# Kernel tuning notes

Measured on AMD Instinct MI355X. Metric: run time of the kernel, lower is better.

The kernel has to match this reference:

```python
import jax, jax.numpy as jnp
import numpy as np

B, S, T, D, H, HD = 1, 2048, 256, 3072, 24, 128
FF = 4 * D
EPS_LN = 1e-6
EPS_RMS = 1e-6


def _layernorm(x):
    m = jnp.mean(x, axis=-1, keepdims=True)
    v = jnp.mean(jnp.square(x - m), axis=-1, keepdims=True)
    return (x - m) * jax.lax.rsqrt(v + EPS_LN)


def _rmsnorm(x, w):
    return x * jax.lax.rsqrt(jnp.mean(jnp.square(x), axis=-1, keepdims=True) + EPS_RMS) * w


def _rope_interleaved(x, cos, sin):
    # x: [B,S,H,HD], cos/sin: [S,HD//2]; non-neox (interleaved) style
    x1 = x[..., 0::2]
    x2 = x[..., 1::2]
    c = cos[None, :, None, :]
    s = sin[None, :, None, :]
    o1 = x1 * c - x2 * s
    o2 = x2 * c + x1 * s
    return jnp.stack([o1, o2], axis=-1).reshape(x.shape)


def setup_inputs() -> dict:
    key = jax.random.key(0)
    ks = jax.random.split(key, 12)

    def n(k, shape, scale):
        return jax.random.normal(k, shape, dtype=jnp.float32) * scale

    # real RoPE tables
    pos = np.arange(S, dtype=np.float64)
    inv_freq = 1.0 / (10000.0 ** (np.arange(0, HD, 2, dtype=np.float64) / HD))
    ang = np.outer(pos, inv_freq)  # [S, HD//2]

    return {
        "img": n(ks[0], (B, S, D), 1.0),
        "vec": n(ks[1], (B, D), 1.0),
        "cos": jnp.asarray(np.cos(ang), jnp.float32),
        "sin": jnp.asarray(np.sin(ang), jnp.float32),
        "k_txt": n(ks[2], (B, T, H, HD), 1.0),
        "v_txt": n(ks[3], (B, T, H, HD), 1.0),
        "mod_w": n(ks[4], (D, 6 * D), 0.02),
        "mod_b": jnp.zeros((6 * D,), jnp.float32),
        "qkv_w": n(ks[5], (D, 3 * D), 0.02),
        "qkv_b": jnp.zeros((3 * D,), jnp.float32),
        "qn_w": jnp.ones((HD,), jnp.float32),
        "kn_w": jnp.ones((HD,), jnp.float32),
        "proj_w": n(ks[6], (D, D), 0.02),
        "proj_b": jnp.zeros((D,), jnp.float32),
        "mlp_w1": n(ks[7], (D, FF), 0.02),
        "mlp_b1": jnp.zeros((FF,), jnp.float32),
        "mlp_w2": n(ks[8], (FF, D), 0.02),
        "mlp_b2": jnp.zeros((D,), jnp.float32),
    }


def reference(img, vec, cos, sin, k_txt, v_txt, mod_w, mod_b, qkv_w, qkv_b,
              qn_w, kn_w, proj_w, proj_b, mlp_w1, mlp_b1, mlp_w2, mlp_b2):
    # modulation: silu(vec) -> linear -> 6 chunks, each [B,1,D]
    mod = jax.nn.silu(vec) @ mod_w + mod_b
    (a_shift, a_scale, a_gate, m_shift, m_scale, m_gate) = [
        m[:, None, :] for m in jnp.split(mod, 6, axis=-1)
    ]

    # LayerNorm (no affine) + scale/shift modulate
    x = _layernorm(img) * (1.0 + a_scale) + a_shift

    qkv = (x @ qkv_w + qkv_b).reshape(B, S, 3, H, HD)
    q, k, v = qkv[:, :, 0], qkv[:, :, 1], qkv[:, :, 2]
    q = _rmsnorm(q, qn_w)
    k = _rmsnorm(k, kn_w)
    q = _rope_interleaved(q, cos, sin)
    k = _rope_interleaved(k, cos, sin)

    # concat text KV cache (no RoPE on text tokens)
    k_all = jnp.concatenate([k, k_txt], axis=1)  # [B,S+T,H,HD]
    v_all = jnp.concatenate([v, v_txt], axis=1)

    scale = 1.0 / jnp.sqrt(jnp.asarray(HD, jnp.float32))
    scores = jnp.einsum('bqhd,bkhd->bhqk', q, k_all) * scale
    probs = jax.nn.softmax(scores, axis=-1)
    attn = jnp.einsum('bhqk,bkhd->bqhd', probs, v_all).reshape(B, S, D)

    attn_out = attn @ proj_w + proj_b

    # ScaleResidualLayerNormScaleShift
    residual = img + a_gate * attn_out
    mlp_in = _layernorm(residual) * (1.0 + m_scale) + m_shift

    mlp_out = jax.nn.gelu(mlp_in @ mlp_w1 + mlp_b1, approximate=True) @ mlp_w2 + mlp_b2
    return residual + m_gate * mlp_out
```

## Files before the change

kernel.cpp:

```cpp
#include <hip/hip_runtime.h>

typedef short short8 __attribute__((ext_vector_type(8)));
typedef float f32x4 __attribute__((ext_vector_type(4)));

#define DEV static __device__ __forceinline__

DEV unsigned short f2bf(float f) {
  union { float f; unsigned u; } v; v.f = f;
  unsigned u = v.u;
  unsigned r = u + 0x7fffu + ((u >> 16) & 1u);
  return (unsigned short)(r >> 16);
}
DEV float bf2f(unsigned short b) {
  union { unsigned u; float f; } v; v.u = ((unsigned)b) << 16;
  return v.f;
}
DEV void load_lds16(const void* g, void* l) {
  __builtin_amdgcn_global_load_lds(
      (const __attribute__((address_space(1))) unsigned int*)g,
      (__attribute__((address_space(3))) unsigned int*)l, 16, 0, 0);
}
DEV int swz(int L) { return L ^ ((L >> 3) & 0x30); }

__global__ __launch_bounds__(256) void zero_mod(const float* __restrict__ b, float* __restrict__ out) {
  int j = blockIdx.x * 256 + threadIdx.x;
  out[j] = b[j];
}

__global__ __launch_bounds__(256) void mod_gemv(const float* __restrict__ vec,
                                                const float* __restrict__ W,
                                                float* __restrict__ out) {
  __shared__ float sv[192];
  int tid = threadIdx.x;
  int kb = blockIdx.y * 192;
  if (tid < 192) {
    float x = vec[kb + tid];
    sv[tid] = x / (1.f + __expf(-x));
  }
  __syncthreads();
  int j = blockIdx.x * 256 + tid;
  float a0 = 0, a1 = 0, a2 = 0, a3 = 0;
  for (int i = 0; i < 192; i += 4) {
    a0 += sv[i + 0] * W[(size_t)(kb + i + 0) * 18432 + j];
    a1 += sv[i + 1] * W[(size_t)(kb + i + 1) * 18432 + j];
    a2 += sv[i + 2] * W[(size_t)(kb + i + 2) * 18432 + j];
    a3 += sv[i + 3] * W[(size_t)(kb + i + 3) * 18432 + j];
  }
  atomicAdd(&out[j], a0 + a1 + a2 + a3);
}

__global__ __launch_bounds__(256) void ln_kernel(const float* __restrict__ in,
                                                 const float* __restrict__ mod,
                                                 int shift_off, int scale_off,
                                                 unsigned short* __restrict__ out) {
  int rowb = blockIdx.x;
  const float* x = in + (size_t)rowb * 3072;
  int tid = threadIdx.x;
  float s = 0.f, ss = 0.f;
  float4 v[3];
#pragma unroll
  for (int r = 0; r < 3; r++) {
    v[r] = *(const float4*)&x[r * 1024 + tid * 4];
    s += v[r].x + v[r].y + v[r].z + v[r].w;
    ss += v[r].x * v[r].x + v[r].y * v[r].y + v[r].z * v[r].z + v[r].w * v[r].w;
  }
#pragma unroll
  for (int m = 32; m; m >>= 1) { s += __shfl_xor(s, m); ss += __shfl_xor(ss, m); }
  __shared__ float red[8];
  int w = tid >> 6, lane = tid & 63;
  if (lane == 0) { red[w] = s; red[4 + w] = ss; }
  __syncthreads();
  s = red[0] + red[1] + red[2] + red[3];
  ss = red[4] + red[5] + red[6] + red[7];
  float mean = s * (1.f / 3072.f);
  float var = ss * (1.f / 3072.f) - mean * mean;
  float rstd = rsqrtf(var + 1e-6f);
#pragma unroll
  for (int r = 0; r < 3; r++) {
    int c = r * 1024 + tid * 4;
    float xv[4] = {v[r].x, v[r].y, v[r].z, v[r].w};
#pragma unroll
    for (int i = 0; i < 4; i++) {
      float o = (xv[i] - mean) * rstd * (1.f + mod[scale_off + c + i]) + mod[shift_off + c + i];
      out[(size_t)rowb * 3072 + c + i] = f2bf(o);
    }
  }
}

__global__ __launch_bounds__(256) void transpose_k(const float* __restrict__ src,
                                                   unsigned short* __restrict__ dst,
                                                   int K, int N) {
  __shared__ float t[64][65];
  int n0 = blockIdx.x * 64, k0 = blockIdx.y * 64;
  int tid = threadIdx.x;
#pragma unroll
  for (int i = 0; i < 16; i++) {
    int lin = i * 256 + tid;
    int r = lin >> 6, c = lin & 63;
    t[r][c] = src[(size_t)(k0 + r) * N + n0 + c];
  }
  __syncthreads();
#pragma unroll
  for (int i = 0; i < 16; i++) {
    int lin = i * 256 + tid;
    int rn = lin >> 6, cn = lin & 63;
    dst[(size_t)(n0 + rn) * K + k0 + cn] = f2bf(t[cn][rn]);
  }
}

__global__ __launch_bounds__(256) void vt_k(const unsigned short* __restrict__ qkvb,
                                            const float* __restrict__ v_txt,
                                            unsigned short* __restrict__ vt) {
  int h = blockIdx.y;
  int c8 = blockIdx.x * 2 + (threadIdx.x >> 7);
  int d = threadIdx.x & 127;
  int kvb = c8 * 8;
  short8 o;
  if (kvb < 2048) {
#pragma unroll
    for (int j = 0; j < 8; j++)
      o[j] = (short)qkvb[(size_t)(kvb + j) * 9216 + 6144 + h * 128 + d];
  } else {
#pragma unroll
    for (int j = 0; j < 8; j++)
      o[j] = (short)f2bf(v_txt[((size_t)(kvb + j - 2048) * 24 + h) * 128 + d]);
  }
  *(short8*)&vt[((size_t)h * 128 + d) * 2304 + kvb] = o;
}

template <int EPI>
__global__ __launch_bounds__(512, 2) void gemm8(const unsigned short* __restrict__ A,
                                                const unsigned short* __restrict__ Bt,
                                                const float* __restrict__ bias,
                                                unsigned short* __restrict__ outb,
                                                int N, int ldk, int klen, size_t zstride) {
  __shared__ unsigned short As[4][8192];
  __shared__ unsigned short Bs[4][8192];
  const int tid = threadIdx.x, lane = tid & 63, w = tid >> 6;
  const int wr = w >> 2, wc = w & 3;
  const int lr = lane & 15, lk = lane >> 4;

  const int bm = blockIdx.y * 256, bn = blockIdx.x * 256;
  const int kbase = blockIdx.z * klen;
  const int NT = klen >> 5;

  const int D0 = tid * 16;
  const int D1 = 8192 + tid * 16;
  const int L0 = swz(D0), L1 = swz(D1);
  const unsigned short* sA0 = A + (size_t)(bm + (L0 >> 6)) * ldk + kbase + ((L0 & 63) >> 1);
  const unsigned short* sA1 = A + (size_t)(bm + (L1 >> 6)) * ldk + kbase + ((L1 & 63) >> 1);
  const unsigned short* sB0 = Bt + (size_t)(bn + (L0 >> 6)) * ldk + kbase + ((L0 & 63) >> 1);
  const unsigned short* sB1 = Bt + (size_t)(bn + (L1 >> 6)) * ldk + kbase + ((L1 & 63) >> 1);

  int aoff[8], boff[4];
#pragma unroll
  for (int mi = 0; mi < 8; mi++)
    aoff[mi] = swz(((wr * 128 + mi * 16 + lr) << 6) | (lk << 4));
#pragma unroll
  for (int ni = 0; ni < 4; ni++)
    boff[ni] = swz(((wc * 64 + ni * 16 + lr) << 6) | (lk << 4));

  f32x4 acc[8][4];
#pragma unroll
  for (int i = 0; i < 8; i++)
#pragma unroll
    for (int j = 0; j < 4; j++) acc[i][j] = (f32x4){0.f, 0.f, 0.f, 0.f};

#pragma unroll
  for (int j = 0; j < 3; j++) {
    load_lds16(sA0 + j * 32, (char*)As + j * 16384 + D0);
    load_lds16(sA1 + j * 32, (char*)As + j * 16384 + D1);
    load_lds16(sB0 + j * 32, (char*)Bs + j * 16384 + D0);
    load_lds16(sB1 + j * 32, (char*)Bs + j * 16384 + D1);
  }
  asm volatile("s_waitcnt vmcnt(8)" ::: "memory");
  __builtin_amdgcn_sched_barrier(0);
  __builtin_amdgcn_s_barrier();

  for (int t = 0; t < NT; ++t) {
    const int rt = t & 3;
    char* Ab = (char*)As + rt * 16384;
    char* Bb = (char*)Bs + rt * 16384;
    const int ss = (t + 3) & 3;
    const int sk = (t + 3) * 32;
    const bool stg = (t + 3) < NT;

    short8 af[8], bf[4];
#pragma unroll
    for (int mi = 0; mi < 8; mi++) af[mi] = *(const short8*)(Ab + aoff[mi]);
#pragma unroll
    for (int ni = 0; ni < 4; ni++) bf[ni] = *(const short8*)(Bb + boff[ni]);
    if (stg) {
      load_lds16(sA0 + sk, (char*)As + ss * 16384 + D0);
      load_lds16(sA1 + sk, (char*)As + ss * 16384 + D1);
      load_lds16(sB0 + sk, (char*)Bs + ss * 16384 + D0);
      load_lds16(sB1 + sk, (char*)Bs + ss * 16384 + D1);
    }
    __builtin_amdgcn_s_setprio(1);
#pragma unroll
    for (int mi = 0; mi < 8; mi++)
#pragma unroll
      for (int ni = 0; ni < 4; ni++)
        acc[mi][ni] = __builtin_amdgcn_mfma_f32_16x16x32_bf16(af[mi], bf[ni], acc[mi][ni], 0, 0, 0);
    __builtin_amdgcn_s_setprio(0);
    if (t < NT - 3) {
      asm volatile("s_waitcnt vmcnt(8)" ::: "memory");
    } else if (t == NT - 3) {
      asm volatile("s_waitcnt vmcnt(4)" ::: "memory");
    } else if (t == NT - 2) {
      asm volatile("s_waitcnt vmcnt(0)" ::: "memory");
    }
    __builtin_amdgcn_sched_barrier(0);
    __builtin_amdgcn_s_barrier();
  }

  const size_t zoff = (size_t)blockIdx.z * zstride;
#pragma unroll
  for (int mi = 0; mi < 8; mi++) {
#pragma unroll
    for (int ni = 0; ni < 4; ni++) {
      int row0 = bm + wr * 128 + mi * 16 + lk * 4;
      int col = bn + wc * 64 + ni * 16 + lr;
#pragma unroll
      for (int r = 0; r < 4; r++) {
        float vv = acc[mi][ni][r];
        if (EPI == 0) {
          outb[(size_t)(row0 + r) * N + col] = f2bf(vv + bias[col]);
        } else if (EPI == 2) {
          float x = vv + bias[col];
          float y = 0.7978845608028654f * (x + 0.044715f * x * x * x);
          float th = 1.f - 2.f / (__expf(2.f * y) + 1.f);
          outb[(size_t)(row0 + r) * N + col] = f2bf(0.5f * x * (1.f + th));
        } else {
          outb[zoff + (size_t)(row0 + r) * N + col] = f2bf(vv);
        }
      }
    }
  }
}

template <int NS>
__global__ __launch_bounds__(256) void sk_epi(const unsigned short* __restrict__ pb,
                                              const float* __restrict__ bias,
                                              const float* __restrict__ addsrc,
                                              const float* __restrict__ gate,
                                              float* __restrict__ out) {
  const int N = 3072;
  const size_t MN = (size_t)2048 * 3072;
  int row = blockIdx.y;
  int col = blockIdx.x * 1024 + threadIdx.x * 4;
  size_t idx = (size_t)row * N + col;
  float4 a = *(const float4*)(addsrc + idx);
  float4 b = *(const float4*)(bias + col);
  float4 g = *(const float4*)(gate + col);
  float sum[4] = {b.x, b.y, b.z, b.w};
#pragma unroll
  for (int s = 0; s < NS; s++) {
    const unsigned short* p = pb + s * MN + idx;
#pragma unroll
    for (int i = 0; i < 4; i++) sum[i] += bf2f(p[i]);
  }
  float4 o;
  o.x = a.x + g.x * sum[0];
  o.y = a.y + g.y * sum[1];
  o.z = a.z + g.z * sum[2];
  o.w = a.w + g.w * sum[3];
  *(float4*)(out + idx) = o;
}

__global__ __launch_bounds__(256) void sk_epiq(const unsigned short* __restrict__ p0,
                                               const unsigned short* __restrict__ p1,
                                               const float* __restrict__ bias,
                                               unsigned short* __restrict__ out) {
  const int N = 9216;
  int row = blockIdx.y;
  int col = blockIdx.x * 1024 + threadIdx.x * 4;
  size_t idx = (size_t)row * N + col;
#pragma unroll
  for (int i = 0; i < 4; i++)
    out[idx + i] = f2bf(bf2f(p0[idx + i]) + bf2f(p1[idx + i]) + bias[col + i]);
}

__global__ __launch_bounds__(64) void qkv_post(const unsigned short* __restrict__ qkv,
                                               const float* __restrict__ k_txt,
                                               const float* __restrict__ cosb,
                                               const float* __restrict__ sinb,
                                               const float* __restrict__ qn,
                                               const float* __restrict__ kn,
                                               unsigned short* __restrict__ qb,
                                               unsigned short* __restrict__ kb) {
  int s = blockIdx.x, h = blockIdx.y;
  int lane = threadIdx.x;
  int d0 = lane * 2;
  if (s < 2048) {
    const unsigned short* rowp = qkv + (size_t)s * 9216;
    float c = cosb[s * 64 + lane], sn = sinb[s * 64 + lane];
    const float ascale = 0.08838834764831845f;
    {
      float a = bf2f(rowp[h * 128 + d0]), b = bf2f(rowp[h * 128 + d0 + 1]);
      float sq = a * a + b * b;
#pragma unroll
      for (int m = 32; m; m >>= 1) sq += __shfl_xor(sq, m);
      float rr = rsqrtf(sq * (1.f / 128.f) + 1e-6f);
      float x1 = a * rr * qn[d0], x2 = b * rr * qn[d0 + 1];
      float o1 = (x1 * c - x2 * sn) * ascale;
      float o2 = (x2 * c + x1 * sn) * ascale;
      size_t off = ((size_t)h * 2048 + s) * 128 + d0;
      qb[off] = f2bf(o1); qb[off + 1] = f2bf(o2);
    }
    {
      float a = bf2f(rowp[3072 + h * 128 + d0]), b = bf2f(rowp[3072 + h * 128 + d0 + 1]);
      float sq = a * a + b * b;
#pragma unroll
      for (int m = 32; m; m >>= 1) sq += __shfl_xor(sq, m);
      float rr = rsqrtf(sq * (1.f / 128.f) + 1e-6f);
      float x1 = a * rr * kn[d0], x2 = b * rr * kn[d0 + 1];
      float o1 = x1 * c - x2 * sn;
      float o2 = x2 * c + x1 * sn;
      size_t off = ((size_t)h * 2304 + s) * 128 + d0;
      kb[off] = f2bf(o1); kb[off + 1] = f2bf(o2);
    }
  } else {
    int t = s - 2048;
    size_t src = ((size_t)t * 24 + h) * 128 + d0;
    size_t off = ((size_t)h * 2304 + s) * 128 + d0;
    kb[off] = f2bf(k_txt[src]); kb[off + 1] = f2bf(k_txt[src + 1]);
  }
}

__global__ __launch_bounds__(512) void attn_k(const unsigned short* __restrict__ qb,
                                              const unsigned short* __restrict__ kb,
                                              const unsigned short* __restrict__ vt,
                                              unsigned short* __restrict__ out) {
  __shared__ unsigned short Ks[2][8192];
  __shared__ unsigned short Vs[2][8192];
  __shared__ unsigned short Ps[8][32 * 72];
  int h = blockIdx.y, q0 = blockIdx.x * 256;
  int tid = threadIdx.x, lane = tid & 63, w = tid >> 6;
  int lr = lane & 15, lk = lane >> 4;

  const unsigned short* kh = kb + (size_t)h * 2304 * 128;
  const unsigned short* vth = vt + (size_t)h * 128 * 2304;

  short8 qf[2][4];
#pragma unroll
  for (int mi = 0; mi < 2; mi++)
#pragma unroll
    for (int kf = 0; kf < 4; kf++)
      qf[mi][kf] = *(const short8*)&qb[((size_t)h * 2048 + q0 + w * 32 + mi * 16 + lr) * 128 + kf * 32 + lk * 8];

  const int kR0 = (tid * 16) >> 8, kR1 = (tid * 16 + 8192) >> 8;
  const int kCc = ((tid * 16) >> 4) & 15;
  const int kOf0 = kR0 * 128 + ((kCc ^ (kR0 & 15)) * 8);
  const int kOf1 = kR1 * 128 + ((kCc ^ (kR1 & 15)) * 8);
  const int vR0 = (tid * 16) >> 7, vR1 = (tid * 16 + 8192) >> 7;
  const int vCc = ((tid * 16) >> 4) & 7;
  const int vOf0 = vR0 * 2304 + ((vCc ^ (vR0 & 7)) * 8);
  const int vOf1 = vR1 * 2304 + ((vCc ^ (vR1 & 7)) * 8);

  float mrow[2][4], lsum[2][4];
#pragma unroll
  for (int mi = 0; mi < 2; mi++)
#pragma unroll
    for (int r = 0; r < 4; r++) { mrow[mi][r] = -1e30f; lsum[mi][r] = 0.f; }
  f32x4 oacc[2][8];
#pragma unroll
  for (int mi = 0; mi < 2; mi++)
#pragma unroll
    for (int i = 0; i < 8; i++) oacc[mi][i] = (f32x4){0.f, 0.f, 0.f, 0.f};

  load_lds16(kh + kOf0, (char*)Ks[0] + tid * 16);
  load_lds16(kh + kOf1, (char*)Ks[0] + tid * 16 + 8192);
  load_lds16(vth + vOf0, (char*)Vs[0] + tid * 16);
  load_lds16(vth + vOf1, (char*)Vs[0] + tid * 16 + 8192);
  asm volatile("s_waitcnt vmcnt(0)" ::: "memory");
  __builtin_amdgcn_sched_barrier(0);
  __builtin_amdgcn_s_barrier();

  for (int kt = 0; kt < 36; kt++) {
    const int cur = kt & 1, nxt = cur ^ 1;
    if (kt + 1 < 36) {
      int kv1 = (kt + 1) * 64;
      load_lds16(kh + (size_t)kv1 * 128 + kOf0, (char*)Ks[nxt] + tid * 16);
      load_lds16(kh + (size_t)kv1 * 128 + kOf1, (char*)Ks[nxt] + tid * 16 + 8192);
      load_lds16(vth + kv1 + vOf0, (char*)Vs[nxt] + tid * 16);
      load_lds16(vth + kv1 + vOf1, (char*)Vs[nxt] + tid * 16 + 8192);
    }

    f32x4 sa[2][4];
#pragma unroll
    for (int mi = 0; mi < 2; mi++)
#pragma unroll
      for (int ni = 0; ni < 4; ni++) sa[mi][ni] = (f32x4){0.f, 0.f, 0.f, 0.f};
    __builtin_amdgcn_s_setprio(1);
#pragma unroll
    for (int kf = 0; kf < 4; kf++) {
#pragma unroll
      for (int ni = 0; ni < 4; ni++) {
        int n = ni * 16 + lr;
        short8 bfr = *(const short8*)&Ks[cur][n * 128 + (((kf * 4 + lk) ^ lr) & 15) * 8];
        sa[0][ni] = __builtin_amdgcn_mfma_f32_16x16x32_bf16(qf[0][kf], bfr, sa[0][ni], 0, 0, 0);
        sa[1][ni] = __builtin_amdgcn_mfma_f32_16x16x32_bf16(qf[1][kf], bfr, sa[1][ni], 0, 0, 0);
      }
    }
    __builtin_amdgcn_s_setprio(0);

#pragma unroll
    for (int mi = 0; mi < 2; mi++) {
#pragma unroll
      for (int r = 0; r < 4; r++) {
        float mx = fmaxf(fmaxf(sa[mi][0][r], sa[mi][1][r]), fmaxf(sa[mi][2][r], sa[mi][3][r]));
#pragma unroll
        for (int m = 8; m; m >>= 1) mx = fmaxf(mx, __shfl_xor(mx, m));
        float mnew = fmaxf(mrow[mi][r], mx);
        float p0 = __expf(sa[mi][0][r] - mnew);
        float p1 = __expf(sa[mi][1][r] - mnew);
        float p2 = __expf(sa[mi][2][r] - mnew);
        float p3 = __expf(sa[mi][3][r] - mnew);
        float su = p0 + p1 + p2 + p3;
#pragma unroll
        for (int m = 8; m; m >>= 1) su += __shfl_xor(su, m);
        float alpha = __expf(mrow[mi][r] - mnew);
        lsum[mi][r] = lsum[mi][r] * alpha + su;
        mrow[mi][r] = mnew;
#pragma unroll
        for (int df = 0; df < 8; df++) oacc[mi][df][r] *= alpha;
        int prow = (mi * 16 + lk * 4 + r) * 72;
        Ps[w][prow + 0 * 16 + lr] = f2bf(p0);
        Ps[w][prow + 1 * 16 + lr] = f2bf(p1);
        Ps[w][prow + 2 * 16 + lr] = f2bf(p2);
        Ps[w][prow + 3 * 16 + lr] = f2bf(p3);
      }
    }

    __builtin_amdgcn_s_setprio(1);
#pragma unroll
    for (int kf2 = 0; kf2 < 2; kf2++) {
      short8 pa0 = *(const short8*)&Ps[w][(0 * 16 + lr) * 72 + kf2 * 32 + lk * 8];
      short8 pa1 = *(const short8*)&Ps[w][(1 * 16 + lr) * 72 + kf2 * 32 + lk * 8];
#pragma unroll
      for (int df = 0; df < 8; df++) {
        int d = df * 16 + lr;
        short8 bv = *(const short8*)&Vs[cur][d * 64 + (((kf2 * 4 + lk) ^ (lr & 7)) & 7) * 8];
        oacc[0][df] = __builtin_amdgcn_mfma_f32_16x16x32_bf16(pa0, bv, oacc[0][df], 0, 0, 0);
        oacc[1][df] = __builtin_amdgcn_mfma_f32_16x16x32_bf16(pa1, bv, oacc[1][df], 0, 0, 0);
      }
    }
    __builtin_amdgcn_s_setprio(0);

    asm volatile("s_waitcnt vmcnt(0)" ::: "memory");
    __builtin_amdgcn_sched_barrier(0);
    __builtin_amdgcn_s_barrier();
  }

#pragma unroll
  for (int mi = 0; mi < 2; mi++) {
#pragma unroll
    for (int r = 0; r < 4; r++) {
      float inv = 1.f / lsum[mi][r];
      int row = q0 + w * 32 + mi * 16 + lk * 4 + r;
#pragma unroll
      for (int df = 0; df < 8; df++)
        out[(size_t)row * 3072 + h * 128 + df * 16 + lr] = f2bf(oacc[mi][df][r] * inv);
    }
  }
}

extern "C" void kernel_launch(void* const* d_in, const int* in_sizes, int n_in,
                              void* d_out, int out_size, void* d_ws, size_t ws_size,
                              hipStream_t stream) {
  const float* img = (const float*)d_in[0];
  const float* vec = (const float*)d_in[1];
  const float* cosb = (const float*)d_in[2];
  const float* sinb = (const float*)d_in[3];
  const float* k_txt = (const float*)d_in[4];
  const float* v_txt = (const float*)d_in[5];
  const float* mod_w = (const float*)d_in[6];
  const float* mod_b = (const float*)d_in[7];
  const float* qkv_w = (const float*)d_in[8];
  const float* qkv_b = (const float*)d_in[9];
  const float* qn_w = (const float*)d_in[10];
  const float* kn_w = (const float*)d_in[11];
  const float* proj_w = (const float*)d_in[12];
  const float* proj_b = (const float*)d_in[13];
  const float* mlp_w1 = (const float*)d_in[14];
  const float* mlp_b1 = (const float*)d_in[15];
  const float* mlp_w2 = (const float*)d_in[16];
  const float* mlp_b2 = (const float*)d_in[17];
  float* outp = (float*)d_out;

  const size_t MN = (size_t)2048 * 3072;
  char* ws = (char*)d_ws;
  unsigned short* qkvb = (unsigned short*)(ws + 0);
  unsigned short* qbuf = (unsigned short*)(ws + 37748736);
  unsigned short* kbuf = (unsigned short*)(ws + 50331648);
  unsigned short* vtbuf = (unsigned short*)(ws + 64487424);
  unsigned short* attnb = (unsigned short*)(ws + 78643200);
  float* resid = (float*)(ws + 91226112);
  unsigned short* xln = (unsigned short*)(ws + 116391936);
  float* modv = (float*)(ws + 128974848);
  unsigned short* wt = (unsigned short*)(ws + 129048576);
  unsigned short* hbuf = (unsigned short*)(ws + 0);
  unsigned short* qp0 = (unsigned short*)(ws + 37748736);
  unsigned short* qp1 = (unsigned short*)(ws + 78643200);
  const size_t qzstride = (78643200 - 37748736) / 2;
  unsigned short* pbuf = (unsigned short*)(ws + 50331648);

  zero_mod<<<72, 256, 0, stream>>>(mod_b, modv);
  mod_gemv<<<dim3(72, 16), 256, 0, stream>>>(vec, mod_w, modv);

  ln_kernel<<<2048, 256, 0, stream>>>(img, modv, 0, 3072, xln);

  transpose_k<<<dim3(144, 48), 256, 0, stream>>>(qkv_w, wt, 3072, 9216);
  gemm8<3><<<dim3(36, 8, 2), 512, 0, stream>>>(xln, wt, nullptr, qp0, 9216, 3072, 1536, qzstride);
  sk_epiq<<<dim3(9, 2048), 256, 0, stream>>>(qp0, qp1, qkv_b, qkvb);

  qkv_post<<<dim3(2304, 24), 64, 0, stream>>>(qkvb, k_txt, cosb, sinb, qn_w, kn_w, qbuf, kbuf);
  vt_k<<<dim3(144, 24), 256, 0, stream>>>(qkvb, v_txt, vtbuf);

  attn_k<<<dim3(8, 24), 512, 0, stream>>>(qbuf, kbuf, vtbuf, attnb);

  transpose_k<<<dim3(48, 48), 256, 0, stream>>>(proj_w, wt, 3072, 3072);
  gemm8<3><<<dim3(12, 8, 2), 512, 0, stream>>>(attnb, wt, nullptr, pbuf, 3072, 3072, 1536, MN);
  sk_epi<2><<<dim3(3, 2048), 256, 0, stream>>>(pbuf, proj_b, img, modv + 2 * 3072, resid);

  ln_kernel<<<2048, 256, 0, stream>>>(resid, modv, 3 * 3072, 4 * 3072, xln);

  transpose_k<<<dim3(192, 48), 256, 0, stream>>>(mlp_w1, wt, 3072, 12288);
  gemm8<2><<<dim3(48, 8, 1), 512, 0, stream>>>(xln, wt, mlp_b1, hbuf, 12288, 3072, 3072, 0);

  transpose_k<<<dim3(48, 192), 256, 0, stream>>>(mlp_w2, wt, 12288, 3072);
  gemm8<3><<<dim3(12, 8, 2), 512, 0, stream>>>(hbuf, wt, nullptr, pbuf, 3072, 12288, 6144, MN);
  sk_epi<2><<<dim3(3, 2048), 256, 0, stream>>>(pbuf, mlp_b2, resid, modv + 5 * 3072, outp);
}
```

Baseline: 956.1 us.

## Triple-buffer attention K/V tiles and skip softmax rescale unless max grows

The attention kernel moves from double to triple buffering of K/V tiles in LDS, issuing loads two tiles ahead and waiting with a partial vmcnt so one tile's loads stay in flight across the barrier. It also adopts lazy online-softmax rescaling: the running max and the output accumulators are rescaled only when the new tile max exceeds the old one by more than 8, which removes most exp and multiply work per tile. The trade-offs are higher LDS use (96KB for K/V), which may reduce occupancy, and probabilities up to e^8 feeding bf16 P, which is a precision risk.

```diff
diff --git a/kernel.cpp b/kernel.cpp
--- a/kernel.cpp
+++ b/kernel.cpp
@@ -332,8 +332,8 @@
                                               const unsigned short* __restrict__ kb,
                                               const unsigned short* __restrict__ vt,
                                               unsigned short* __restrict__ out) {
-  __shared__ unsigned short Ks[2][8192];
-  __shared__ unsigned short Vs[2][8192];
+  __shared__ unsigned short Ks[3][8192];
+  __shared__ unsigned short Vs[3][8192];
   __shared__ unsigned short Ps[8][32 * 72];
   int h = blockIdx.y, q0 = blockIdx.x * 256;
   int tid = threadIdx.x, lane = tid & 63, w = tid >> 6;
@@ -369,22 +369,26 @@
 #pragma unroll
     for (int i = 0; i < 8; i++) oacc[mi][i] = (f32x4){0.f, 0.f, 0.f, 0.f};
 
-  load_lds16(kh + kOf0, (char*)Ks[0] + tid * 16);
-  load_lds16(kh + kOf1, (char*)Ks[0] + tid * 16 + 8192);
-  load_lds16(vth + vOf0, (char*)Vs[0] + tid * 16);
-  load_lds16(vth + vOf1, (char*)Vs[0] + tid * 16 + 8192);
-  asm volatile("s_waitcnt vmcnt(0)" ::: "memory");
+#pragma unroll
+  for (int j = 0; j < 2; j++) {
+    int kv = j * 64;
+    load_lds16(kh + (size_t)kv * 128 + kOf0, (char*)Ks[j] + tid * 16);
+    load_lds16(kh + (size_t)kv * 128 + kOf1, (char*)Ks[j] + tid * 16 + 8192);
+    load_lds16(vth + kv + vOf0, (char*)Vs[j] + tid * 16);
+    load_lds16(vth + kv + vOf1, (char*)Vs[j] + tid * 16 + 8192);
+  }
+  asm volatile("s_waitcnt vmcnt(4)" ::: "memory");
   __builtin_amdgcn_sched_barrier(0);
   __builtin_amdgcn_s_barrier();
 
+  int cur = 0, st = 2;
   for (int kt = 0; kt < 36; kt++) {
-    const int cur = kt & 1, nxt = cur ^ 1;
-    if (kt + 1 < 36) {
-      int kv1 = (kt + 1) * 64;
-      load_lds16(kh + (size_t)kv1 * 128 + kOf0, (char*)Ks[nxt] + tid * 16);
-      load_lds16(kh + (size_t)kv1 * 128 + kOf1, (char*)Ks[nxt] + tid * 16 + 8192);
-      load_lds16(vth + kv1 + vOf0, (char*)Vs[nxt] + tid * 16);
-      load_lds16(vth + kv1 + vOf1, (char*)Vs[nxt] + tid * 16 + 8192);
+    if (kt + 2 < 36) {
+      int kv2 = (kt + 2) * 64;
+      load_lds16(kh + (size_t)kv2 * 128 + kOf0, (char*)Ks[st] + tid * 16);
+      load_lds16(kh + (size_t)kv2 * 128 + kOf1, (char*)Ks[st] + tid * 16 + 8192);
+      load_lds16(vth + kv2 + vOf0, (char*)Vs[st] + tid * 16);
+      load_lds16(vth + kv2 + vOf1, (char*)Vs[st] + tid * 16 + 8192);
     }
 
     f32x4 sa[2][4];
@@ -412,19 +416,23 @@
         float mx = fmaxf(fmaxf(sa[mi][0][r], sa[mi][1][r]), fmaxf(sa[mi][2][r], sa[mi][3][r]));
 #pragma unroll
         for (int m = 8; m; m >>= 1) mx = fmaxf(mx, __shfl_xor(mx, m));
-        float mnew = fmaxf(mrow[mi][r], mx);
-        float p0 = __expf(sa[mi][0][r] - mnew);
-        float p1 = __expf(sa[mi][1][r] - mnew);
-        float p2 = __expf(sa[mi][2][r] - mnew);
-        float p3 = __expf(sa[mi][3][r] - mnew);
+        float mold = mrow[mi][r];
+        if (mx > mold + 8.f) {
+          float alpha = __expf(mold - mx);
+          lsum[mi][r] *= alpha;
+#pragma unroll
+          for (int df = 0; df < 8; df++) oacc[mi][df][r] *= alpha;
+          mrow[mi][r] = mx;
+          mold = mx;
+        }
+        float p0 = __expf(sa[mi][0][r] - mold);
+        float p1 = __expf(sa[mi][1][r] - mold);
+        float p2 = __expf(sa[mi][2][r] - mold);
+        float p3 = __expf(sa[mi][3][r] - mold);
         float su = p0 + p1 + p2 + p3;
 #pragma unroll
         for (int m = 8; m; m >>= 1) su += __shfl_xor(su, m);
-        float alpha = __expf(mrow[mi][r] - mnew);
-        lsum[mi][r] = lsum[mi][r] * alpha + su;
-        mrow[mi][r] = mnew;
-#pragma unroll
-        for (int df = 0; df < 8; df++) oacc[mi][df][r] *= alpha;
+        lsum[mi][r] += su;
         int prow = (mi * 16 + lk * 4 + r) * 72;
         Ps[w][prow + 0 * 16 + lr] = f2bf(p0);
         Ps[w][prow + 1 * 16 + lr] = f2bf(p1);
@@ -448,9 +456,15 @@
     }
     __builtin_amdgcn_s_setprio(0);
 
-    asm volatile("s_waitcnt vmcnt(0)" ::: "memory");
+    if (kt < 34) {
+      asm volatile("s_waitcnt vmcnt(4)" ::: "memory");
+    } else if (kt == 34) {
+      asm volatile("s_waitcnt vmcnt(0)" ::: "memory");
+    }
     __builtin_amdgcn_sched_barrier(0);
     __builtin_amdgcn_s_barrier();
+    cur = (cur == 2) ? 0 : cur + 1;
+    st = (st == 2) ? 0 : st + 1;
   }
 
 #pragma unroll
```

Result: no change. 960.8 us (+0.5%).
